# Kernel tuning notes

Hardware: AMD Instinct MI355X
Metric: run time of the kernel (lower is better)

The kernel has to match this reference:

```python
import jax, jax.numpy as jnp
import numpy as np
from jax import lax

B_, L_, D_ = 4, 2048, 256
DI, NS, DC, DTR = 512, 16, 4, 16  # d_inner=2*D, d_state, d_conv, dt_rank=ceil(D/16)
DFF = 4 * D_


def setup_inputs():
    key = jax.random.key(0)
    ks = jax.random.split(key, 20)
    rn = lambda k, s, sc=0.02: jax.random.normal(k, s, jnp.float32) * sc
    return {
        "x": jax.random.normal(ks[0], (B_, L_, D_), jnp.float32),
        "in_proj_w": rn(ks[1], (2 * DI, D_)), "in_proj_b": jnp.zeros((2 * DI,), jnp.float32),
        "conv_w": rn(ks[2], (DI, DC), 0.1), "conv_b": jnp.zeros((DI,), jnp.float32),
        "x_proj_w": rn(ks[3], (DTR + 2 * NS, DI)),
        "dt_proj_w": rn(ks[4], (DI, DTR), 0.1), "dt_proj_b": rn(ks[5], (DI,), 0.5),
        "A_log": jnp.log(jnp.tile(jnp.arange(1, NS + 1, dtype=jnp.float32), (DI, 1))),
        "D_ssm": jnp.ones((DI,), jnp.float32),
        "out_proj_w": rn(ks[6], (D_, DI)), "out_proj_b": jnp.zeros((D_,), jnp.float32),
        "ln1_g": jnp.ones((D_,), jnp.float32), "ln1_b": jnp.zeros((D_,), jnp.float32),
        "fc1_w": rn(ks[7], (DFF, D_)), "fc1_b": jnp.zeros((DFF,), jnp.float32),
        "fc2_w": rn(ks[8], (D_, DFF)), "fc2_b": jnp.zeros((D_,), jnp.float32),
        "ln2_g": jnp.ones((D_,), jnp.float32), "ln2_b": jnp.zeros((D_,), jnp.float32),
    }


def _layer_norm(x, g, b, eps=1e-5):
    m = jnp.mean(x, -1, keepdims=True)
    v = jnp.mean((x - m) ** 2, -1, keepdims=True)
    return (x - m) / jnp.sqrt(v + eps) * g + b


def _mamba(x, in_proj_w, in_proj_b, conv_w, conv_b, x_proj_w, dt_proj_w, dt_proj_b, A_log, D_ssm, out_proj_w, out_proj_b):
    B, L, D = x.shape
    xz = x @ in_proj_w.T + in_proj_b                       # [B,L,2*DI]
    xi, z = jnp.split(xz, 2, axis=-1)
    # causal depthwise conv over time
    xc = jnp.transpose(xi, (0, 2, 1))                       # [B,DI,L]
    xc = lax.conv_general_dilated(xc, conv_w[:, None, :], (1,), [(DC - 1, 0)],
                                  dimension_numbers=("NCH", "OIH", "NCH"),
                                  feature_group_count=DI)
    xi = jax.nn.silu(jnp.transpose(xc + conv_b[None, :, None], (0, 2, 1)))  # [B,L,DI]
    x_dbl = xi @ x_proj_w.T                                 # [B,L,DTR+2*NS]
    dt, Bs, Cs = jnp.split(x_dbl, [DTR, DTR + NS], axis=-1)
    dt = jax.nn.softplus(dt @ dt_proj_w.T + dt_proj_b)      # [B,L,DI]
    A = -jnp.exp(A_log)                                     # [DI,NS]
    dA = jnp.exp(dt[..., None] * A)                         # [B,L,DI,NS]
    dBu = dt[..., None] * Bs[:, :, None, :] * xi[..., None]  # [B,L,DI,NS]
    dA_t = jnp.moveaxis(dA, 1, 0)
    dBu_t = jnp.moveaxis(dBu, 1, 0)
    C_t = jnp.moveaxis(Cs, 1, 0)                            # [L,B,NS]

    def step(h, inp):
        a, bu, c = inp
        h = a * h + bu                                      # [B,DI,NS]
        y = jnp.einsum("bdn,bn->bd", h, c)
        return h, y

    h0 = jnp.zeros((B, DI, NS), x.dtype)
    _, ys = lax.scan(step, h0, (dA_t, dBu_t, C_t))
    y = jnp.moveaxis(ys, 0, 1) + xi * D_ssm                 # [B,L,DI]
    y = y * jax.nn.silu(z)
    return y @ out_proj_w.T + out_proj_b


def reference(x, in_proj_w, in_proj_b, conv_w, conv_b, x_proj_w, dt_proj_w, dt_proj_b,
              A_log, D_ssm, out_proj_w, out_proj_b, ln1_g, ln1_b, fc1_w, fc1_b,
              fc2_w, fc2_b, ln2_g, ln2_b):
    gelu = lambda t: jax.nn.gelu(t, approximate=False)
    ssm = _mamba(x, in_proj_w, in_proj_b, conv_w, conv_b, x_proj_w, dt_proj_w,
                 dt_proj_b, A_log, D_ssm, out_proj_w, out_proj_b)
    y = _layer_norm(x + ssm, ln1_g, ln1_b)                  # dropout = identity (eval)
    ffn = gelu(gelu(y @ fc1_w.T + fc1_b) @ fc2_w.T + fc2_b)
    return _layer_norm(y + ffn, ln2_g, ln2_b)
```

## Files before the change

### kernel.cpp

```cpp
#include <hip/hip_runtime.h>

typedef __bf16 bf16x8 __attribute__((ext_vector_type(8)));
typedef float  f32x4  __attribute__((ext_vector_type(4)));

#define AS1 __attribute__((address_space(1)))
#define AS3 __attribute__((address_space(3)))

__device__ __forceinline__ float bf2f(ushort u) {
    union { unsigned int i; float f; } v; v.i = ((unsigned int)u) << 16; return v.f;
}
__device__ __forceinline__ ushort f2bf(float f) {
    union { float f; unsigned int i; } v; v.f = f;
    unsigned int i = v.i;
    unsigned int r = i + 0x7FFFu + ((i >> 16) & 1u);
    return (ushort)(r >> 16);
}
__device__ __forceinline__ float bflo(unsigned int u) { return bf2f((ushort)(u & 0xFFFFu)); }
__device__ __forceinline__ float bfhi(unsigned int u) { return bf2f((ushort)(u >> 16)); }

__global__ void sniff_k(const ushort* __restrict__ x, int* __restrict__ flag)
{
    const int lane = threadIdx.x;
    int cnt = 0;
    #pragma unroll
    for (int r = 0; r < 4; r++) {
        const ushort u = x[lane + r * 64];
        const int e = (u >> 7) & 0xFF;
        if ((u & 0x7FFF) == 0 || (e >= 112 && e <= 141)) cnt++;
    }
    #pragma unroll
    for (int o = 32; o > 0; o >>= 1) cnt += __shfl_down(cnt, o);
    if (lane == 0) flag[0] = (cnt >= 224) ? 1 : 0;
}

struct CanonArgs {
    const void* src[20];
    int off[20];
    int total;
};

__launch_bounds__(256)
__global__ void canon_k(CanonArgs a, ushort* __restrict__ dst, const int* __restrict__ flag)
{
    const int i = blockIdx.x * 256 + threadIdx.x;
    if (i >= a.total) return;
    const int fl = flag[0];
    int s = 0;
    #pragma unroll
    for (int t = 1; t < 20; t++) if (i >= a.off[t]) s = t;
    const int li = i - a.off[s];
    ushort v;
    if (fl) v = ((const ushort*)a.src[s])[li];
    else    v = f2bf(((const float*)a.src[s])[li]);
    dst[i] = v;
}

__launch_bounds__(256)
__global__ void prep_k(const ushort* __restrict__ dtw, const ushort* __restrict__ xpw,
                       ushort* __restrict__ dtw_pad, ushort* __restrict__ xpw_pad)
{
    const int i = blockIdx.x * 256 + threadIdx.x;
    if (i < 16384) {
        const int dd = i >> 5, r = i & 31;
        dtw_pad[i] = (r < 16) ? dtw[dd * 16 + r] : (ushort)0;
    } else {
        const int j = i - 16384;
        const int r = j >> 9;
        xpw_pad[j] = (r < 48) ? xpw[j] : (ushort)0;
    }
}

template<int BM, int BN, int ACT, bool HASB, bool WF32, bool WBF16>
__launch_bounds__(256, 2)
__global__ void gemm_bt(const ushort* __restrict__ A, const ushort* __restrict__ W,
                        const ushort* __restrict__ bias,
                        float* __restrict__ Cf, ushort* __restrict__ Cb,
                        int M, int N, int K, int lda)
{
    constexpr int WMT = BM / 32;
    constexpr int WNT = BN / 32;
    __shared__ __align__(16) ushort As[BM * 32];
    __shared__ __align__(16) ushort Bs[BN * 32];
    const int tid  = threadIdx.x;
    const int wave = tid >> 6;
    const int lane = tid & 63;
    const int m0 = blockIdx.x * BM;
    const int n0 = blockIdx.y * BN;
    const int wm = (wave >> 1) * (BM / 2);
    const int wn = (wave & 1) * (BN / 2);
    const int lrow = lane & 15;
    const int quad = lane >> 4;

    f32x4 acc[WMT][WNT];
    #pragma unroll
    for (int i = 0; i < WMT; i++)
        #pragma unroll
        for (int j = 0; j < WNT; j++)
            #pragma unroll
            for (int r = 0; r < 4; r++) acc[i][j][r] = 0.f;

    for (int k0 = 0; k0 < K; k0 += 32) {
        #pragma unroll
        for (int t = 0; t < BM / 64; t++) {
            const int inst = t * 4 + wave;
            const int row  = inst * 16 + (lane >> 2);
            const int sub  = lane & 3;
            const ushort* gp = A + (size_t)(m0 + row) * lda + (k0 + sub * 8);
            __builtin_amdgcn_global_load_lds((AS1 void*)(void*)gp,
                                             (AS3 void*)(As + inst * 512), 16, 0, 0);
        }
        #pragma unroll
        for (int t = 0; t < BN / 64; t++) {
            const int inst = t * 4 + wave;
            const int row  = inst * 16 + (lane >> 2);
            const int sub  = lane & 3;
            const ushort* gp = W + (size_t)(n0 + row) * K + (k0 + sub * 8);
            __builtin_amdgcn_global_load_lds((AS1 void*)(void*)gp,
                                             (AS3 void*)(Bs + inst * 512), 16, 0, 0);
        }
        __syncthreads();

        bf16x8 afr[WMT], bfr[WNT];
        #pragma unroll
        for (int i = 0; i < WMT; i++)
            afr[i] = *(const bf16x8*)&As[(wm + i * 16 + lrow) * 32 + quad * 8];
        #pragma unroll
        for (int j = 0; j < WNT; j++)
            bfr[j] = *(const bf16x8*)&Bs[(wn + j * 16 + lrow) * 32 + quad * 8];
        #pragma unroll
        for (int i = 0; i < WMT; i++)
            #pragma unroll
            for (int j = 0; j < WNT; j++)
                acc[i][j] = __builtin_amdgcn_mfma_f32_16x16x32_bf16(afr[i], bfr[j], acc[i][j], 0, 0, 0);
        __syncthreads();
    }

    #pragma unroll
    for (int i = 0; i < WMT; i++) {
        const int gm = m0 + wm + i * 16 + quad * 4;
        #pragma unroll
        for (int j = 0; j < WNT; j++) {
            const int gn = n0 + wn + j * 16 + lrow;
            const float bv = HASB ? bf2f(bias[gn]) : 0.f;
            #pragma unroll
            for (int r = 0; r < 4; r++) {
                float v = acc[i][j][r] + bv;
                if (ACT == 1) v = 0.5f * v * (1.f + erff(v * 0.70710678118654752f));
                if (ACT == 2) v = (v > 15.f) ? v : __logf(1.f + __expf(v));
                const size_t off = (size_t)(gm + r) * N + gn;
                if (WF32)  Cf[off] = v;
                if (WBF16) Cb[off] = f2bf(v);
            }
        }
    }
}

__launch_bounds__(256)
__global__ void conv_silu_k(const ushort* __restrict__ xz, const ushort* __restrict__ cw,
                            const ushort* __restrict__ cb, ushort* __restrict__ xc)
{
    const int idx = blockIdx.x * 256 + threadIdx.x;
    const int t  = idx >> 6;
    const int d8 = (idx & 63) * 8;
    const int l  = t & 2047;

    ushort wl[32];
    *(uint4*)&wl[0]  = *(const uint4*)&cw[d8 * 4];
    *(uint4*)&wl[8]  = *(const uint4*)&cw[d8 * 4 + 8];
    *(uint4*)&wl[16] = *(const uint4*)&cw[d8 * 4 + 16];
    *(uint4*)&wl[24] = *(const uint4*)&cw[d8 * 4 + 24];

    ushort bl[8];
    *(uint4*)&bl[0] = *(const uint4*)&cb[d8];

    float acc[8];
    #pragma unroll
    for (int j = 0; j < 8; j++) acc[j] = bf2f(bl[j]);

    #pragma unroll
    for (int k = 0; k < 4; k++) {
        const int ls = l - 3 + k;
        if (ls >= 0) {
            ushort xl[8];
            *(uint4*)&xl[0] = *(const uint4*)&xz[(size_t)(t - 3 + k) * 1024 + d8];
            #pragma unroll
            for (int j = 0; j < 8; j++) acc[j] += bf2f(xl[j]) * bf2f(wl[j * 4 + k]);
        }
    }
    ushort ol[8];
    #pragma unroll
    for (int j = 0; j < 8; j++) {
        const float s = acc[j] / (1.f + __expf(-acc[j]));
        ol[j] = f2bf(s);
    }
    *(uint4*)&xc[(size_t)idx * 8] = *(uint4*)&ol[0];
}

__launch_bounds__(256)
__global__ void scan1_k(const float* __restrict__ dt, const ushort* __restrict__ xc,
                        const float* __restrict__ xdbl, const ushort* __restrict__ Alog,
                        float* __restrict__ summ)
{
    __shared__ float Bsh[32 * 16];
    const int tid = threadIdx.x;
    const int c = blockIdx.y, b = blockIdx.z;
    const int t0 = b * 2048 + c * 32;
    for (int e = tid; e < 512; e += 256)
        Bsh[e] = xdbl[(size_t)(t0 + (e >> 4)) * 64 + 16 + (e & 15)];
    __syncthreads();
    const int d = blockIdx.x * 256 + tid;
    float A[16], h[16];
    #pragma unroll
    for (int n = 0; n < 16; n++) {
        A[n] = -__expf(bf2f(Alog[d * 16 + n]));
        h[n] = 0.f;
    }
    float sdt = 0.f;
    for (int i = 0; i < 32; i++) {
        const int t = t0 + i;
        const float dtv = dt[(size_t)t * 512 + d];
        const float xiv = bf2f(xc[(size_t)t * 512 + d]);
        const float dx = dtv * xiv;
        sdt += dtv;
        const float* Br = &Bsh[i * 16];
        #pragma unroll
        for (int n = 0; n < 16; n++) {
            const float da = __expf(dtv * A[n]);
            h[n] = da * h[n] + dx * Br[n];
        }
    }
    const size_t base = ((size_t)(b * 64 + c) * 32) * 512 + d;
    #pragma unroll
    for (int n = 0; n < 16; n++) summ[base + (size_t)n * 512] = __expf(A[n] * sdt);
    #pragma unroll
    for (int n = 0; n < 16; n++) summ[base + (size_t)(16 + n) * 512] = h[n];
}

__launch_bounds__(512)
__global__ void combine_k(float* __restrict__ summ)
{
    const int b = blockIdx.x >> 4, n = blockIdx.x & 15;
    const int d = threadIdx.x;
    float h = 0.f;
    for (int c = 0; c < 64; c++) {
        const size_t sb = ((size_t)((b * 64 + c) * 32 + n)) * 512 + d;
        const float p  = summ[sb];
        const float hl = summ[sb + 8192];
        summ[sb] = h;
        h = p * h + hl;
    }
}

__launch_bounds__(256)
__global__ void scan2_k(const float* __restrict__ dt, ushort* xc,
                        const float* __restrict__ xdbl, const ushort* __restrict__ Alog,
                        const float* __restrict__ summ, const ushort* __restrict__ xz,
                        const ushort* __restrict__ Dssm)
{
    __shared__ float Bsh[32 * 16];
    __shared__ float Csh[32 * 16];
    const int tid = threadIdx.x;
    const int c = blockIdx.y, b = blockIdx.z;
    const int t0 = b * 2048 + c * 32;
    for (int e = tid; e < 512; e += 256) {
        const size_t rb = (size_t)(t0 + (e >> 4)) * 64 + (e & 15);
        Bsh[e] = xdbl[rb + 16];
        Csh[e] = xdbl[rb + 32];
    }
    __syncthreads();
    const int d = blockIdx.x * 256 + tid;
    float A[16], h[16];
    #pragma unroll
    for (int n = 0; n < 16; n++) A[n] = -__expf(bf2f(Alog[d * 16 + n]));
    const size_t base = ((size_t)(b * 64 + c) * 32) * 512 + d;
    #pragma unroll
    for (int n = 0; n < 16; n++) h[n] = summ[base + (size_t)n * 512];
    const float Dv = bf2f(Dssm[d]);
    for (int i = 0; i < 32; i++) {
        const int t = t0 + i;
        const float dtv = dt[(size_t)t * 512 + d];
        const float xiv = bf2f(xc[(size_t)t * 512 + d]);
        const float dx = dtv * xiv;
        const float* Br = &Bsh[i * 16];
        const float* Cr = &Csh[i * 16];
        float yv = 0.f;
        #pragma unroll
        for (int n = 0; n < 16; n++) {
            const float da = __expf(dtv * A[n]);
            h[n] = da * h[n] + dx * Br[n];
            yv += h[n] * Cr[n];
        }
        yv += xiv * Dv;
        const float zv = bf2f(xz[(size_t)t * 1024 + 512 + d]);
        yv *= zv / (1.f + __expf(-zv));
        xc[(size_t)t * 512 + d] = f2bf(yv);
    }
}

__launch_bounds__(256)
__global__ void ln1_k(const void* __restrict__ xin, const float* __restrict__ sout,
                      const ushort* __restrict__ g, const ushort* __restrict__ bb,
                      float* __restrict__ y1f, ushort* __restrict__ y1b,
                      const int* __restrict__ flag)
{
    const int w = threadIdx.x >> 6, l = threadIdx.x & 63;
    const int t = blockIdx.x * 4 + w;
    const size_t base = (size_t)t * 256 + l * 4;
    const int fl = flag[0];
    float v[4];
    if (fl) {
        const uint2 xr = *(const uint2*)((const ushort*)xin + base);
        v[0] = bflo(xr.x); v[1] = bfhi(xr.x); v[2] = bflo(xr.y); v[3] = bfhi(xr.y);
    } else {
        const float4 xr = *(const float4*)((const float*)xin + base);
        v[0] = xr.x; v[1] = xr.y; v[2] = xr.z; v[3] = xr.w;
    }
    const float4 sv = *(const float4*)&sout[base];
    v[0] += sv.x; v[1] += sv.y; v[2] += sv.z; v[3] += sv.w;
    float s = v[0] + v[1] + v[2] + v[3];
    #pragma unroll
    for (int o = 32; o > 0; o >>= 1) s += __shfl_xor(s, o);
    const float mean = s * (1.f / 256.f);
    float q = 0.f;
    #pragma unroll
    for (int j = 0; j < 4; j++) { const float dv = v[j] - mean; q += dv * dv; }
    #pragma unroll
    for (int o = 32; o > 0; o >>= 1) q += __shfl_xor(q, o);
    const float r = rsqrtf(q * (1.f / 256.f) + 1e-5f);
    const uint2 gv = *(const uint2*)&g[l * 4];
    const uint2 bv = *(const uint2*)&bb[l * 4];
    const float gf[4] = { bflo(gv.x), bfhi(gv.x), bflo(gv.y), bfhi(gv.y) };
    const float bf[4] = { bflo(bv.x), bfhi(bv.x), bflo(bv.y), bfhi(bv.y) };
    float4 of;
    float* op = (float*)&of;
    ushort ob[4];
    #pragma unroll
    for (int j = 0; j < 4; j++) {
        const float o2 = (v[j] - mean) * r * gf[j] + bf[j];
        op[j] = o2; ob[j] = f2bf(o2);
    }
    *(float4*)&y1f[base] = of;
    *(uint2*)&y1b[base] = *(uint2*)&ob[0];
}

__launch_bounds__(256)
__global__ void ln2_k(const float* __restrict__ y1f, const float* __restrict__ ffn,
                      const ushort* __restrict__ g, const ushort* __restrict__ bb,
                      void* __restrict__ out, const int* __restrict__ flag)
{
    const int w = threadIdx.x >> 6, l = threadIdx.x & 63;
    const int t = blockIdx.x * 4 + w;
    const size_t base = (size_t)t * 256 + l * 4;
    const int fl = flag[0];
    const float4 av = *(const float4*)&y1f[base];
    const float4 fv = *(const float4*)&ffn[base];
    float v[4] = { av.x + fv.x, av.y + fv.y, av.z + fv.z, av.w + fv.w };
    float s = v[0] + v[1] + v[2] + v[3];
    #pragma unroll
    for (int o = 32; o > 0; o >>= 1) s += __shfl_xor(s, o);
    const float mean = s * (1.f / 256.f);
    float q = 0.f;
    #pragma unroll
    for (int j = 0; j < 4; j++) { const float dv = v[j] - mean; q += dv * dv; }
    #pragma unroll
    for (int o = 32; o > 0; o >>= 1) q += __shfl_xor(q, o);
    const float r = rsqrtf(q * (1.f / 256.f) + 1e-5f);
    const uint2 gv = *(const uint2*)&g[l * 4];
    const uint2 bv = *(const uint2*)&bb[l * 4];
    const float gf[4] = { bflo(gv.x), bfhi(gv.x), bflo(gv.y), bfhi(gv.y) };
    const float bf[4] = { bflo(bv.x), bfhi(bv.x), bflo(bv.y), bfhi(bv.y) };
    if (fl) {
        ushort ob[4];
        #pragma unroll
        for (int j = 0; j < 4; j++) ob[j] = f2bf((v[j] - mean) * r * gf[j] + bf[j]);
        *(uint2*)((ushort*)out + base) = *(uint2*)&ob[0];
    } else {
        float4 of;
        float* op = (float*)&of;
        #pragma unroll
        for (int j = 0; j < 4; j++) op[j] = (v[j] - mean) * r * gf[j] + bf[j];
        *(float4*)((float*)out + base) = of;
    }
}

extern "C" void kernel_launch(void* const* d_in, const int* in_sizes, int n_in,
                              void* d_out, int out_size, void* d_ws, size_t ws_size,
                              hipStream_t stream)
{
    char* ws = (char*)d_ws;
    int*    flag  = (int*)(ws + 0);
    ushort* canon = (ushort*)(ws + 256);

    static const int coff[20] = {
        0,        2097152,  2359296,  2360320,  2362368,
        2362880,  2387456,  2395648,  2396160,  2404352,
        2404864,  2535936,  2536192,  2536448,  2536704,
        2798848,  2799872,  3062016,  3062272,  3062528 };
    static const int ctot = 3062784;

    CanonArgs ca;
    for (int i = 0; i < 20; i++) { ca.src[i] = d_in[i]; ca.off[i] = coff[i]; }
    ca.total = ctot;

    const ushort* cx   = canon + coff[0];
    const ushort* cipw = canon + coff[1];
    const ushort* cipb = canon + coff[2];
    const ushort* ccw  = canon + coff[3];
    const ushort* ccb  = canon + coff[4];
    const ushort* cxpw = canon + coff[5];
    const ushort* cdtw = canon + coff[6];
    const ushort* cdtb = canon + coff[7];
    const ushort* calog= canon + coff[8];
    const ushort* cdssm= canon + coff[9];
    const ushort* copw = canon + coff[10];
    const ushort* copb = canon + coff[11];
    const ushort* cln1g= canon + coff[12];
    const ushort* cln1b= canon + coff[13];
    const ushort* cf1w = canon + coff[14];
    const ushort* cf1b = canon + coff[15];
    const ushort* cf2w = canon + coff[16];
    const ushort* cf2b = canon + coff[17];
    const ushort* cln2g= canon + coff[18];
    const ushort* cln2b= canon + coff[19];

    ushort* xpw_pad = (ushort*)(ws + 6291456);
    ushort* dtw_pad = (ushort*)(ws + 6356992);
    ushort* xz      = (ushort*)(ws + 8388608);
    ushort* xc      = (ushort*)(ws + 25165824);
    float*  xdbl_f  = (float*)(ws + 33554432);
    ushort* xdbl_b  = (ushort*)(ws + 35651584);
    float*  dt      = (float*)(ws + 36700160);
    float*  summ    = (float*)(ws + 53477376);
    float*  sout = (float*)(ws + 8388608);
    float*  y1f  = (float*)(ws + 16777216);
    ushort* y1b  = (ushort*)(ws + 33554432);
    ushort* f1   = (ushort*)(ws + 37748736);
    float*  ffn  = (float*)(ws + 54525952);
    ushort* yb   = xc;

    sniff_k<<<1, 64, 0, stream>>>((const ushort*)d_in[0], flag);
    canon_k<<<(ctot + 255) / 256, 256, 0, stream>>>(ca, canon, flag);
    prep_k<<<192, 256, 0, stream>>>(cdtw, cxpw, dtw_pad, xpw_pad);

    gemm_bt<128, 128, 0, true, false, true><<<dim3(64, 8), 256, 0, stream>>>(
        cx, cipw, cipb, nullptr, xz, 8192, 1024, 256, 256);
    conv_silu_k<<<2048, 256, 0, stream>>>(xz, ccw, ccb, xc);
    gemm_bt<64, 64, 0, false, true, true><<<dim3(128, 1), 256, 0, stream>>>(
        xc, xpw_pad, nullptr, xdbl_f, xdbl_b, 8192, 64, 512, 512);
    gemm_bt<128, 64, 2, true, true, false><<<dim3(64, 8), 256, 0, stream>>>(
        xdbl_b, dtw_pad, cdtb, dt, nullptr, 8192, 512, 32, 64);
    scan1_k<<<dim3(2, 64, 4), 256, 0, stream>>>(dt, xc, xdbl_f, calog, summ);
    combine_k<<<64, 512, 0, stream>>>(summ);
    scan2_k<<<dim3(2, 64, 4), 256, 0, stream>>>(dt, xc, xdbl_f, calog, summ, xz, cdssm);
    gemm_bt<128, 64, 0, true, true, false><<<dim3(64, 4), 256, 0, stream>>>(
        yb, copw, copb, sout, nullptr, 8192, 256, 512, 512);
    ln1_k<<<2048, 256, 0, stream>>>(d_in[0], sout, cln1g, cln1b, y1f, y1b, flag);
    gemm_bt<128, 128, 1, true, false, true><<<dim3(64, 8), 256, 0, stream>>>(
        y1b, cf1w, cf1b, nullptr, f1, 8192, 1024, 256, 256);
    gemm_bt<128, 64, 1, true, true, false><<<dim3(64, 4), 256, 0, stream>>>(
        f1, cf2w, cf2b, ffn, nullptr, 8192, 256, 1024, 1024);
    ln2_k<<<2048, 256, 0, stream>>>(y1f, ffn, cln2g, cln2b, d_out, flag);
}
```

Before: 268.3 us.

## Fuse dt projection and softplus into scan kernels, split-K x_proj, drop sniff/prep kernels

Removes the separate dt_proj GEMM and its fp32 dt buffer by recomputing dt = softplus(x_dbl[:16]·W + b) per timestep inside both scan passes. The x_proj GEMM is replaced by a dedicated split-K kernel with two K halves that the scans sum on load. The dtype sniff is inlined into each consumer kernel and the padding prep kernel is folded into canon_k, which cuts three launches. In exchange the 16-term dot product is computed twice, once per scan pass, and every thread redundantly reads the sniff samples.

```diff
diff --git a/kernel.cpp b/kernel.cpp
--- a/kernel.cpp
+++ b/kernel.cpp
@@ -18,9 +18,8 @@
 __device__ __forceinline__ float bflo(unsigned int u) { return bf2f((ushort)(u & 0xFFFFu)); }
 __device__ __forceinline__ float bfhi(unsigned int u) { return bf2f((ushort)(u >> 16)); }
 
-__global__ void sniff_k(const ushort* __restrict__ x, int* __restrict__ flag)
-{
-    const int lane = threadIdx.x;
+__device__ __forceinline__ bool sniff_inline(const ushort* __restrict__ x) {
+    const int lane = threadIdx.x & 63;
     int cnt = 0;
     #pragma unroll
     for (int r = 0; r < 4; r++) {
@@ -29,8 +28,8 @@
         if ((u & 0x7FFF) == 0 || (e >= 112 && e <= 141)) cnt++;
     }
     #pragma unroll
-    for (int o = 32; o > 0; o >>= 1) cnt += __shfl_down(cnt, o);
-    if (lane == 0) flag[0] = (cnt >= 224) ? 1 : 0;
+    for (int o = 32; o > 0; o >>= 1) cnt += __shfl_xor(cnt, o);
+    return cnt >= 224;
 }
 
 struct CanonArgs {
@@ -40,11 +39,16 @@
 };
 
 __launch_bounds__(256)
-__global__ void canon_k(CanonArgs a, ushort* __restrict__ dst, const int* __restrict__ flag)
+__global__ void canon_k(CanonArgs a, ushort* __restrict__ dst, ushort* __restrict__ xpw_pad,
+                        const ushort* __restrict__ sniffx)
 {
     const int i = blockIdx.x * 256 + threadIdx.x;
-    if (i >= a.total) return;
-    const int fl = flag[0];
+    if (i >= a.total) {
+        const int j = i - a.total;
+        if (j < 8192) xpw_pad[24576 + j] = 0;
+        return;
+    }
+    const bool fl = sniff_inline(sniffx);
     int s = 0;
     #pragma unroll
     for (int t = 1; t < 20; t++) if (i >= a.off[t]) s = t;
@@ -53,21 +57,7 @@
     if (fl) v = ((const ushort*)a.src[s])[li];
     else    v = f2bf(((const float*)a.src[s])[li]);
     dst[i] = v;
-}
-
-__launch_bounds__(256)
-__global__ void prep_k(const ushort* __restrict__ dtw, const ushort* __restrict__ xpw,
-                       ushort* __restrict__ dtw_pad, ushort* __restrict__ xpw_pad)
-{
-    const int i = blockIdx.x * 256 + threadIdx.x;
-    if (i < 16384) {
-        const int dd = i >> 5, r = i & 31;
-        dtw_pad[i] = (r < 16) ? dtw[dd * 16 + r] : (ushort)0;
-    } else {
-        const int j = i - 16384;
-        const int r = j >> 9;
-        xpw_pad[j] = (r < 48) ? xpw[j] : (ushort)0;
-    }
+    if (s == 5) xpw_pad[li] = v;
 }
 
 template<int BM, int BN, int ACT, bool HASB, bool WF32, bool WBF16>
@@ -146,11 +136,79 @@
             for (int r = 0; r < 4; r++) {
                 float v = acc[i][j][r] + bv;
                 if (ACT == 1) v = 0.5f * v * (1.f + erff(v * 0.70710678118654752f));
-                if (ACT == 2) v = (v > 15.f) ? v : __logf(1.f + __expf(v));
                 const size_t off = (size_t)(gm + r) * N + gn;
                 if (WF32)  Cf[off] = v;
                 if (WBF16) Cb[off] = f2bf(v);
             }
+        }
+    }
+}
+
+__launch_bounds__(256, 2)
+__global__ void xdbl_k(const ushort* __restrict__ A, const ushort* __restrict__ W,
+                       float* __restrict__ Cf)
+{
+    __shared__ __align__(16) ushort As[64 * 32];
+    __shared__ __align__(16) ushort Bs[64 * 32];
+    const int tid  = threadIdx.x;
+    const int wave = tid >> 6;
+    const int lane = tid & 63;
+    const int m0   = blockIdx.x * 64;
+    const int kbeg = blockIdx.y * 256;
+    const int wm = (wave >> 1) * 32;
+    const int wn = (wave & 1) * 32;
+    const int lrow = lane & 15;
+    const int quad = lane >> 4;
+
+    f32x4 acc[2][2];
+    #pragma unroll
+    for (int i = 0; i < 2; i++)
+        #pragma unroll
+        for (int j = 0; j < 2; j++)
+            #pragma unroll
+            for (int r = 0; r < 4; r++) acc[i][j][r] = 0.f;
+
+    for (int k0 = kbeg; k0 < kbeg + 256; k0 += 32) {
+        {
+            const int row = wave * 16 + (lane >> 2);
+            const int sub = lane & 3;
+            const ushort* gp = A + (size_t)(m0 + row) * 512 + (k0 + sub * 8);
+            __builtin_amdgcn_global_load_lds((AS1 void*)(void*)gp,
+                                             (AS3 void*)(As + wave * 512), 16, 0, 0);
+        }
+        {
+            const int row = wave * 16 + (lane >> 2);
+            const int sub = lane & 3;
+            const ushort* gp = W + (size_t)row * 512 + (k0 + sub * 8);
+            __builtin_amdgcn_global_load_lds((AS1 void*)(void*)gp,
+                                             (AS3 void*)(Bs + wave * 512), 16, 0, 0);
+        }
+        __syncthreads();
+        bf16x8 afr[2], bfr[2];
+        #pragma unroll
+        for (int i = 0; i < 2; i++)
+            afr[i] = *(const bf16x8*)&As[(wm + i * 16 + lrow) * 32 + quad * 8];
+        #pragma unroll
+        for (int j = 0; j < 2; j++)
+            bfr[j] = *(const bf16x8*)&Bs[(wn + j * 16 + lrow) * 32 + quad * 8];
+        #pragma unroll
+        for (int i = 0; i < 2; i++)
+            #pragma unroll
+            for (int j = 0; j < 2; j++)
+                acc[i][j] = __builtin_amdgcn_mfma_f32_16x16x32_bf16(afr[i], bfr[j], acc[i][j], 0, 0, 0);
+        __syncthreads();
+    }
+
+    float* out = Cf + (size_t)blockIdx.y * 524288;
+    #pragma unroll
+    for (int i = 0; i < 2; i++) {
+        const int gm = m0 + wm + i * 16 + quad * 4;
+        #pragma unroll
+        for (int j = 0; j < 2; j++) {
+            const int gn = wn + j * 16 + lrow;
+            #pragma unroll
+            for (int r = 0; r < 4; r++)
+                out[(size_t)(gm + r) * 64 + gn] = acc[i][j][r];
         }
     }
 }
@@ -197,18 +255,29 @@
 }
 
 __launch_bounds__(256)
-__global__ void scan1_k(const float* __restrict__ dt, const ushort* __restrict__ xc,
-                        const float* __restrict__ xdbl, const ushort* __restrict__ Alog,
-                        float* __restrict__ summ)
-{
-    __shared__ float Bsh[32 * 16];
+__global__ void scan1_k(const float* __restrict__ xdbl, const ushort* __restrict__ xc,
+                        const ushort* __restrict__ dtw, const ushort* __restrict__ dtb,
+                        const ushort* __restrict__ Alog, float* __restrict__ summ)
+{
+    __shared__ float XD[32 * 32];
     const int tid = threadIdx.x;
     const int c = blockIdx.y, b = blockIdx.z;
     const int t0 = b * 2048 + c * 32;
-    for (int e = tid; e < 512; e += 256)
-        Bsh[e] = xdbl[(size_t)(t0 + (e >> 4)) * 64 + 16 + (e & 15)];
+    for (int e = tid; e < 1024; e += 256) {
+        const size_t idx = (size_t)(t0 + (e >> 5)) * 64 + (e & 31);
+        XD[e] = xdbl[idx] + xdbl[idx + 524288];
+    }
     __syncthreads();
     const int d = blockIdx.x * 256 + tid;
+
+    const uint4 w0 = *(const uint4*)&dtw[d * 16];
+    const uint4 w1 = *(const uint4*)&dtw[d * 16 + 8];
+    const float wd[16] = { bflo(w0.x), bfhi(w0.x), bflo(w0.y), bfhi(w0.y),
+                           bflo(w0.z), bfhi(w0.z), bflo(w0.w), bfhi(w0.w),
+                           bflo(w1.x), bfhi(w1.x), bflo(w1.y), bfhi(w1.y),
+                           bflo(w1.z), bfhi(w1.z), bflo(w1.w), bfhi(w1.w) };
+    const float dtbv = bf2f(dtb[d]);
+
     float A[16], h[16];
     #pragma unroll
     for (int n = 0; n < 16; n++) {
@@ -218,15 +287,18 @@
     float sdt = 0.f;
     for (int i = 0; i < 32; i++) {
         const int t = t0 + i;
-        const float dtv = dt[(size_t)t * 512 + d];
+        const float* Xr = &XD[i * 32];
+        float s = dtbv;
+        #pragma unroll
+        for (int k = 0; k < 16; k++) s += Xr[k] * wd[k];
+        const float dtv = (s > 15.f) ? s : __logf(1.f + __expf(s));
         const float xiv = bf2f(xc[(size_t)t * 512 + d]);
         const float dx = dtv * xiv;
         sdt += dtv;
-        const float* Br = &Bsh[i * 16];
         #pragma unroll
         for (int n = 0; n < 16; n++) {
             const float da = __expf(dtv * A[n]);
-            h[n] = da * h[n] + dx * Br[n];
+            h[n] = da * h[n] + dx * Xr[16 + n];
         }
     }
     const size_t base = ((size_t)(b * 64 + c) * 32) * 512 + d;
@@ -252,23 +324,30 @@
 }
 
 __launch_bounds__(256)
-__global__ void scan2_k(const float* __restrict__ dt, ushort* xc,
-                        const float* __restrict__ xdbl, const ushort* __restrict__ Alog,
-                        const float* __restrict__ summ, const ushort* __restrict__ xz,
-                        const ushort* __restrict__ Dssm)
-{
-    __shared__ float Bsh[32 * 16];
-    __shared__ float Csh[32 * 16];
+__global__ void scan2_k(const float* __restrict__ xdbl, ushort* xc,
+                        const ushort* __restrict__ dtw, const ushort* __restrict__ dtb,
+                        const ushort* __restrict__ Alog, const float* __restrict__ summ,
+                        const ushort* __restrict__ xz, const ushort* __restrict__ Dssm)
+{
+    __shared__ float XD[32 * 48];
     const int tid = threadIdx.x;
     const int c = blockIdx.y, b = blockIdx.z;
     const int t0 = b * 2048 + c * 32;
-    for (int e = tid; e < 512; e += 256) {
-        const size_t rb = (size_t)(t0 + (e >> 4)) * 64 + (e & 15);
-        Bsh[e] = xdbl[rb + 16];
-        Csh[e] = xdbl[rb + 32];
+    for (int e = tid; e < 1536; e += 256) {
+        const size_t idx = (size_t)(t0 + (e / 48)) * 64 + (e % 48);
+        XD[e] = xdbl[idx] + xdbl[idx + 524288];
     }
     __syncthreads();
     const int d = blockIdx.x * 256 + tid;
+
+    const uint4 w0 = *(const uint4*)&dtw[d * 16];
+    const uint4 w1 = *(const uint4*)&dtw[d * 16 + 8];
+    const float wd[16] = { bflo(w0.x), bfhi(w0.x), bflo(w0.y), bfhi(w0.y),
+                           bflo(w0.z), bfhi(w0.z), bflo(w0.w), bfhi(w0.w),
+                           bflo(w1.x), bfhi(w1.x), bflo(w1.y), bfhi(w1.y),
+                           bflo(w1.z), bfhi(w1.z), bflo(w1.w), bfhi(w1.w) };
+    const float dtbv = bf2f(dtb[d]);
+
     float A[16], h[16];
     #pragma unroll
     for (int n = 0; n < 16; n++) A[n] = -__expf(bf2f(Alog[d * 16 + n]));
@@ -276,19 +355,22 @@
     #pragma unroll
     for (int n = 0; n < 16; n++) h[n] = summ[base + (size_t)n * 512];
     const float Dv = bf2f(Dssm[d]);
+
     for (int i = 0; i < 32; i++) {
         const int t = t0 + i;
-        const float dtv = dt[(size_t)t * 512 + d];
+        const float* Xr = &XD[i * 48];
+        float s = dtbv;
+        #pragma unroll
+        for (int k = 0; k < 16; k++) s += Xr[k] * wd[k];
+        const float dtv = (s > 15.f) ? s : __logf(1.f + __expf(s));
         const float xiv = bf2f(xc[(size_t)t * 512 + d]);
         const float dx = dtv * xiv;
-        const float* Br = &Bsh[i * 16];
-        const float* Cr = &Csh[i * 16];
         float yv = 0.f;
         #pragma unroll
         for (int n = 0; n < 16; n++) {
             const float da = __expf(dtv * A[n]);
-            h[n] = da * h[n] + dx * Br[n];
-            yv += h[n] * Cr[n];
+            h[n] = da * h[n] + dx * Xr[16 + n];
+            yv += h[n] * Xr[32 + n];
         }
         yv += xiv * Dv;
         const float zv = bf2f(xz[(size_t)t * 1024 + 512 + d]);
@@ -301,12 +383,12 @@
 __global__ void ln1_k(const void* __restrict__ xin, const float* __restrict__ sout,
                       const ushort* __restrict__ g, const ushort* __restrict__ bb,
                       float* __restrict__ y1f, ushort* __restrict__ y1b,
-                      const int* __restrict__ flag)
+                      const ushort* __restrict__ sniffx)
 {
     const int w = threadIdx.x >> 6, l = threadIdx.x & 63;
     const int t = blockIdx.x * 4 + w;
     const size_t base = (size_t)t * 256 + l * 4;
-    const int fl = flag[0];
+    const bool fl = sniff_inline(sniffx);
     float v[4];
     if (fl) {
         const uint2 xr = *(const uint2*)((const ushort*)xin + base);
@@ -346,12 +428,12 @@
 __launch_bounds__(256)
 __global__ void ln2_k(const float* __restrict__ y1f, const float* __restrict__ ffn,
                       const ushort* __restrict__ g, const ushort* __restrict__ bb,
-                      void* __restrict__ out, const int* __restrict__ flag)
+                      void* __restrict__ out, const ushort* __restrict__ sniffx)
 {
     const int w = threadIdx.x >> 6, l = threadIdx.x & 63;
     const int t = blockIdx.x * 4 + w;
     const size_t base = (size_t)t * 256 + l * 4;
-    const int fl = flag[0];
+    const bool fl = sniff_inline(sniffx);
     const float4 av = *(const float4*)&y1f[base];
     const float4 fv = *(const float4*)&ffn[base];
     float v[4] = { av.x + fv.x, av.y + fv.y, av.z + fv.z, av.w + fv.w };
@@ -388,7 +470,6 @@
                               hipStream_t stream)
 {
     char* ws = (char*)d_ws;
-    int*    flag  = (int*)(ws + 0);
     ushort* canon = (ushort*)(ws + 256);
 
     static const int coff[20] = {
@@ -407,7 +488,6 @@
     const ushort* cipb = canon + coff[2];
     const ushort* ccw  = canon + coff[3];
     const ushort* ccb  = canon + coff[4];
-    const ushort* cxpw = canon + coff[5];
     const ushort* cdtw = canon + coff[6];
     const ushort* cdtb = canon + coff[7];
     const ushort* calog= canon + coff[8];
@@ -424,40 +504,32 @@
     const ushort* cln2b= canon + coff[19];
 
     ushort* xpw_pad = (ushort*)(ws + 6291456);
-    ushort* dtw_pad = (ushort*)(ws + 6356992);
     ushort* xz      = (ushort*)(ws + 8388608);
     ushort* xc      = (ushort*)(ws + 25165824);
-    float*  xdbl_f  = (float*)(ws + 33554432);
-    ushort* xdbl_b  = (ushort*)(ws + 35651584);
-    float*  dt      = (float*)(ws + 36700160);
-    float*  summ    = (float*)(ws + 53477376);
-    float*  sout = (float*)(ws + 8388608);
-    float*  y1f  = (float*)(ws + 16777216);
-    ushort* y1b  = (ushort*)(ws + 33554432);
-    ushort* f1   = (ushort*)(ws + 37748736);
-    float*  ffn  = (float*)(ws + 54525952);
-    ushort* yb   = xc;
-
-    sniff_k<<<1, 64, 0, stream>>>((const ushort*)d_in[0], flag);
-    canon_k<<<(ctot + 255) / 256, 256, 0, stream>>>(ca, canon, flag);
-    prep_k<<<192, 256, 0, stream>>>(cdtw, cxpw, dtw_pad, xpw_pad);
-
+    float*  xdbl    = (float*)(ws + 33554432);
+    float*  summ    = (float*)(ws + 37748736);
+    float*  sout    = (float*)(ws + 53477376);
+    float*  y1f     = (float*)(ws + 61865984);
+    ushort* y1b     = (ushort*)(ws + 70254592);
+    ushort* f1      = (ushort*)(ws + 74448896);
+    float*  ffn     = (float*)(ws + 91226112);
+    ushort* yb      = xc;
+    const ushort* sx = (const ushort*)d_in[0];
+
+    canon_k<<<(ctot + 8192 + 255) / 256, 256, 0, stream>>>(ca, canon, xpw_pad, sx);
     gemm_bt<128, 128, 0, true, false, true><<<dim3(64, 8), 256, 0, stream>>>(
         cx, cipw, cipb, nullptr, xz, 8192, 1024, 256, 256);
     conv_silu_k<<<2048, 256, 0, stream>>>(xz, ccw, ccb, xc);
-    gemm_bt<64, 64, 0, false, true, true><<<dim3(128, 1), 256, 0, stream>>>(
-        xc, xpw_pad, nullptr, xdbl_f, xdbl_b, 8192, 64, 512, 512);
-    gemm_bt<128, 64, 2, true, true, false><<<dim3(64, 8), 256, 0, stream>>>(
-        xdbl_b, dtw_pad, cdtb, dt, nullptr, 8192, 512, 32, 64);
-    scan1_k<<<dim3(2, 64, 4), 256, 0, stream>>>(dt, xc, xdbl_f, calog, summ);
+    xdbl_k<<<dim3(128, 2), 256, 0, stream>>>(xc, xpw_pad, xdbl);
+    scan1_k<<<dim3(2, 64, 4), 256, 0, stream>>>(xdbl, xc, cdtw, cdtb, calog, summ);
     combine_k<<<64, 512, 0, stream>>>(summ);
-    scan2_k<<<dim3(2, 64, 4), 256, 0, stream>>>(dt, xc, xdbl_f, calog, summ, xz, cdssm);
+    scan2_k<<<dim3(2, 64, 4), 256, 0, stream>>>(xdbl, xc, cdtw, cdtb, calog, summ, xz, cdssm);
     gemm_bt<128, 64, 0, true, true, false><<<dim3(64, 4), 256, 0, stream>>>(
         yb, copw, copb, sout, nullptr, 8192, 256, 512, 512);
-    ln1_k<<<2048, 256, 0, stream>>>(d_in[0], sout, cln1g, cln1b, y1f, y1b, flag);
+    ln1_k<<<2048, 256, 0, stream>>>(d_in[0], sout, cln1g, cln1b, y1f, y1b, sx);
     gemm_bt<128, 128, 1, true, false, true><<<dim3(64, 8), 256, 0, stream>>>(
         y1b, cf1w, cf1b, nullptr, f1, 8192, 1024, 256, 256);
     gemm_bt<128, 64, 1, true, true, false><<<dim3(64, 4), 256, 0, stream>>>(
         f1, cf2w, cf2b, ffn, nullptr, 8192, 256, 1024, 1024);
-    ln2_k<<<2048, 256, 0, stream>>>(y1f, ffn, cln2g, cln2b, d_out, flag);
-}
+    ln2_k<<<2048, 256, 0, stream>>>(y1f, ffn, cln2g, cln2b, d_out, sx);
+}
```

New measurement: 271.6 us. No clear change (+1.2%).
